# Performance work log

Hardware: AMD Instinct MI355X
Metric: run time of the kernel (lower is better)

## Reference

```python
import jax, jax.numpy as jnp
import numpy as np

K = 6            # kmer length
NF = 8192        # n_filters (> 4**K so kmer_params has shape (NF, 4, K))
M = 4 ** K       # 4096 kmers
B = 1024         # batch


def setup_inputs() -> dict:
    key = jax.random.key(0)
    k1, k2 = jax.random.split(key)
    freq = jax.random.uniform(k1, (B, M), dtype=jnp.float32)          # kmer frequencies (B, 4^k)
    kmer_params = jax.random.normal(k2, (NF, 4, K), dtype=jnp.float32)
    temperature = jnp.ones((1,), dtype=jnp.float32)
    # base-4 digits of arange(4^k), most-significant first == itertools.product order
    pos = 4 ** jnp.arange(K - 1, -1, -1)
    kmer_idcs = ((jnp.arange(M)[:, None] // pos[None, :]) % 4).astype(jnp.int32)  # (M, K)
    return {"freq": freq, "kmer_params": kmer_params,
            "temperature": temperature, "kmer_idcs": kmer_idcs}


def reference(freq, kmer_params, temperature, kmer_idcs):
    k = kmer_params.shape[-1]
    # matches[f, i] = sum_j kmer_params[f, kmer_idcs[i, j], j]
    # Advanced indexing broadcasts (M, k) indices against arange(k): result (F, M, k).
    # This replaces torch's expand-to-(F, M, 1, k) + gather + squeeze + sum(-1).
    matches = kmer_params[:, kmer_idcs, jnp.arange(k)].sum(axis=-1)   # (F, M)
    probs = jax.nn.softmax(matches / temperature, axis=1)             # softmax over kmers
    pooled = freq @ probs.T                                           # (B, F)
    profile = pooled / pooled.sum(axis=1, keepdims=True)
    return profile
```

## Files before the change

kernel.cpp:

```cpp
#include <hip/hip_runtime.h>


typedef __bf16  bf16x8 __attribute__((ext_vector_type(8)));
typedef float   f32x4  __attribute__((ext_vector_type(4)));

#define GLD16(gp, lp)                                                          \
  __builtin_amdgcn_global_load_lds(                                            \
      (const __attribute__((address_space(1))) void*)(gp),                     \
      (__attribute__((address_space(3))) void*)(lp), 16, 0, 0)

__device__ __forceinline__ short f2bf(float x) {
  unsigned u = __float_as_uint(x);
  unsigned r = (u + 0x7fffu + ((u >> 16) & 1u)) >> 16;
  return (short)r;
}

__device__ __forceinline__ float wave_max(float v) {
  #pragma unroll
  for (int off = 32; off; off >>= 1) v = fmaxf(v, __shfl_xor(v, off, 64));
  return v;
}
__device__ __forceinline__ float wave_sum(float v) {
  #pragma unroll
  for (int off = 32; off; off >>= 1) v += __shfl_xor(v, off, 64);
  return v;
}

__global__ __launch_bounds__(256) void cast_kernel(const float* __restrict__ in,
                                                   short* __restrict__ out) {
  int idx = blockIdx.x * 256 + threadIdx.x;
  float4 v = ((const float4*)in)[idx];
  short4 o;
  o.x = f2bf(v.x); o.y = f2bf(v.y); o.z = f2bf(v.z); o.w = f2bf(v.w);
  ((short4*)out)[idx] = o;
}

__global__ __launch_bounds__(256) void tables_kernel(const float* __restrict__ kp,
                                                     const float* __restrict__ temp,
                                                     float* __restrict__ E1t,
                                                     float* __restrict__ E2) {
  const int t = threadIdx.x;
  const int lane = t & 63, wave = t >> 6;
  const int f = blockIdx.x * 4 + wave;
  const float* P = kp + f * 24;
  const int d0 = (lane >> 4) & 3, d1 = (lane >> 2) & 3, d2 = lane & 3;
  const float thi = P[d0 * 6 + 0] + P[d1 * 6 + 1] + P[d2 * 6 + 2];
  const float tlo = P[d0 * 6 + 3] + P[d1 * 6 + 4] + P[d2 * 6 + 5];
  const float mxhi = wave_max(thi), mxlo = wave_max(tlo);
  const float invT = 1.0f / temp[0];
  const float e1 = __expf((thi - mxhi) * invT);
  const float e2 = __expf((tlo - mxlo) * invT);
  const float s1 = wave_sum(e1), s2 = wave_sum(e2);
  const float invZ = 1.0f / (s1 * s2);
  E1t[lane * 8192 + f] = e1 * invZ;
  E2[(size_t)f * 64 + lane] = e2;
}

__global__ __launch_bounds__(256, 2) void gemm_kernel(const short* __restrict__ A,
                                                      const float* __restrict__ E1t,
                                                      const float* __restrict__ E2,
                                                      float* __restrict__ C) {
  __shared__ short As[2][64 * 64];

  const int t = threadIdx.x;
  const int lane = t & 63, wave = t >> 6;
  const int quad = lane >> 4, l16 = lane & 15;
  const int m0 = blockIdx.y * 64;
  const int n0 = blockIdx.x * 256;
  const int wn = wave * 64;

  f32x4 acc[4][4];
  #pragma unroll
  for (int i = 0; i < 4; i++)
    #pragma unroll
    for (int j = 0; j < 4; j++) acc[i][j] = (f32x4){0.f, 0.f, 0.f, 0.f};

  int nrow[4];
  #pragma unroll
  for (int j = 0; j < 4; j++) nrow[j] = n0 + wn + j * 16 + l16;
  bf16x8 e2f[2][4];
  #pragma unroll
  for (int j = 0; j < 4; j++)
    #pragma unroll
    for (int ks = 0; ks < 2; ks++) {
      const float* p = E2 + (size_t)nrow[j] * 64 + (ks * 4 + quad) * 8;
      float4 lo = *(const float4*)p, hi = *(const float4*)(p + 4);
      bf16x8 bb;
      bb[0] = (__bf16)lo.x; bb[1] = (__bf16)lo.y;
      bb[2] = (__bf16)lo.z; bb[3] = (__bf16)lo.w;
      bb[4] = (__bf16)hi.x; bb[5] = (__bf16)hi.y;
      bb[6] = (__bf16)hi.z; bb[7] = (__bf16)hi.w;
      e2f[ks][j] = bb;
    }

  const int lane_row = lane >> 3;
  const int src_col = ((lane & 7) ^ lane_row) * 8;
  const int sw = l16 & 7;
  const int chunk = wave * 2;
  const short* Abase = A + (size_t)(m0 + lane_row) * 4096 + src_col;

  #define STG(kt, buf) do {                                                    \
    GLD16(Abase + (size_t)((chunk + 0) * 8) * 4096 + (kt) * 64,                \
          &As[buf][(chunk + 0) * 512 + lane * 8]);                             \
    GLD16(Abase + (size_t)((chunk + 1) * 8) * 4096 + (kt) * 64,                \
          &As[buf][(chunk + 1) * 512 + lane * 8]);                             \
  } while (0)

  STG(0, 0);
  float e1n[4], e1c[4];
  #pragma unroll
  for (int j = 0; j < 4; j++) e1n[j] = E1t[nrow[j]];

  const f32x4 Z4 = (f32x4){0.f, 0.f, 0.f, 0.f};

  #pragma unroll 1
  for (int kt = 0; kt < 64; ++kt) {
    const int cb = kt & 1;
    const int tn = (kt + 1 > 63) ? 63 : kt + 1;

    STG(tn, cb ^ 1);
    #pragma unroll
    for (int j = 0; j < 4; j++) e1c[j] = e1n[j];
    #pragma unroll
    for (int j = 0; j < 4; j++) e1n[j] = E1t[tn * 8192 + nrow[j]];

    asm volatile("s_waitcnt vmcnt(6)" ::: "memory");
    __builtin_amdgcn_s_barrier();

    bf16x8 a[4][2];
    #pragma unroll
    for (int i = 0; i < 4; i++)
      #pragma unroll
      for (int ks = 0; ks < 2; ks++)
        a[i][ks] = *(const bf16x8*)&As[cb][(i * 16 + l16) * 64 +
                                          (((ks * 4 + quad) ^ sw) * 8)];

    __builtin_amdgcn_s_setprio(1);
    #pragma unroll
    for (int j = 0; j < 4; j++) {
      const f32x4 s4 = (f32x4){e1c[j], e1c[j], e1c[j], e1c[j]};
      #pragma unroll
      for (int i = 0; i < 4; i++) {
        f32x4 P = __builtin_amdgcn_mfma_f32_16x16x32_bf16(a[i][0], e2f[0][j], Z4, 0, 0, 0);
        P = __builtin_amdgcn_mfma_f32_16x16x32_bf16(a[i][1], e2f[1][j], P, 0, 0, 0);
        acc[i][j] += s4 * P;
      }
    }
    __builtin_amdgcn_s_setprio(0);
    __builtin_amdgcn_s_barrier();
  }

  asm volatile("s_waitcnt vmcnt(0)" ::: "memory");

  #pragma unroll
  for (int i = 0; i < 4; i++) {
    #pragma unroll
    for (int r = 0; r < 4; r++) {
      const int brow = m0 + i * 16 + quad * 4 + r;
      float* crow = C + (size_t)brow * 8192 + n0 + wn + l16;
      #pragma unroll
      for (int j = 0; j < 4; j++) crow[j * 16] = acc[i][j][r];
    }
  }
  #undef STG
}

__global__ __launch_bounds__(256) void norm_kernel(float* __restrict__ out) {
  const int b = blockIdx.x;
  const int t = threadIdx.x;
  const int lane = t & 63, wave = t >> 6;
  __shared__ float red[4];

  float4* row = (float4*)(out + (size_t)b * 8192);
  float4 v[8];
  float s = 0.0f;
  #pragma unroll
  for (int q = 0; q < 8; q++) {
    v[q] = row[q * 256 + t];
    s += (v[q].x + v[q].y) + (v[q].z + v[q].w);
  }
  float ws = wave_sum(s);
  if (lane == 0) red[wave] = ws;
  __syncthreads();
  float tot = (red[0] + red[1]) + (red[2] + red[3]);
  float inv = 1.0f / tot;
  #pragma unroll
  for (int q = 0; q < 8; q++) {
    v[q].x *= inv; v[q].y *= inv; v[q].z *= inv; v[q].w *= inv;
    row[q * 256 + t] = v[q];
  }
}

extern "C" void kernel_launch(void* const* d_in, const int* in_sizes, int n_in,
                              void* d_out, int out_size, void* d_ws, size_t ws_size,
                              hipStream_t stream) {
  const float* freq    = (const float*)d_in[0];
  const float* kparams = (const float*)d_in[1];
  const float* temp    = (const float*)d_in[2];

  float* out = (float*)d_out;

  short* freqb = (short*)d_ws;
  float* E1t   = (float*)(freqb + (size_t)1024 * 4096);
  float* E2    = E1t + (size_t)64 * 8192;

  cast_kernel  <<<4096, 256, 0, stream>>>(freq, freqb);
  tables_kernel<<<2048, 256, 0, stream>>>(kparams, temp, E1t, E2);
  gemm_kernel  <<<dim3(32, 16), 256, 0, stream>>>(freqb, E1t, E2, out);
  norm_kernel  <<<1024, 256, 0, stream>>>(out);
}
```

Measured before the change: 159.3 us.

## Merge prep kernels and retile GEMM to register-direct loads with smaller tiles

Fuses the bf16 cast and softmax-table kernels into one launch, which removes one launch and its inter-kernel gap. The GEMM drops LDS staging and barriers. Each wave now loads its own 16-row A fragment straight from global memory into registers, with a one-step register prefetch. Tiles shrink from 64x256 to 64x64 per block, with a swizzled block index for L2 locality and launch bounds raised to 4 blocks per CU. This trades LDS reuse of A across waves for more blocks, higher occupancy and no syncs, at the cost of more redundant global loads of A and E2.

```diff
diff --git a/kernel.cpp b/kernel.cpp
--- a/kernel.cpp
+++ b/kernel.cpp
@@ -3,11 +3,6 @@
 
 typedef __bf16  bf16x8 __attribute__((ext_vector_type(8)));
 typedef float   f32x4  __attribute__((ext_vector_type(4)));
-
-#define GLD16(gp, lp)                                                          \
-  __builtin_amdgcn_global_load_lds(                                            \
-      (const __attribute__((address_space(1))) void*)(gp),                     \
-      (__attribute__((address_space(3))) void*)(lp), 16, 0, 0)
 
 __device__ __forceinline__ short f2bf(float x) {
   unsigned u = __float_as_uint(x);
@@ -26,64 +21,61 @@
   return v;
 }
 
-__global__ __launch_bounds__(256) void cast_kernel(const float* __restrict__ in,
-                                                   short* __restrict__ out) {
-  int idx = blockIdx.x * 256 + threadIdx.x;
-  float4 v = ((const float4*)in)[idx];
-  short4 o;
-  o.x = f2bf(v.x); o.y = f2bf(v.y); o.z = f2bf(v.z); o.w = f2bf(v.w);
-  ((short4*)out)[idx] = o;
+__global__ __launch_bounds__(256) void prep_kernel(const float* __restrict__ freq,
+                                                   short* __restrict__ freqb,
+                                                   const float* __restrict__ kp,
+                                                   const float* __restrict__ temp,
+                                                   float* __restrict__ E1t,
+                                                   float* __restrict__ E2) {
+  if (blockIdx.x < 4096) {
+    int idx = blockIdx.x * 256 + threadIdx.x;
+    float4 v = ((const float4*)freq)[idx];
+    short4 o;
+    o.x = f2bf(v.x); o.y = f2bf(v.y); o.z = f2bf(v.z); o.w = f2bf(v.w);
+    ((short4*)freqb)[idx] = o;
+  } else {
+    const int t = threadIdx.x;
+    const int lane = t & 63, wave = t >> 6;
+    const int f = (blockIdx.x - 4096) * 4 + wave;
+    const float* P = kp + f * 24;
+    const int d0 = (lane >> 4) & 3, d1 = (lane >> 2) & 3, d2 = lane & 3;
+    const float thi = P[d0 * 6 + 0] + P[d1 * 6 + 1] + P[d2 * 6 + 2];
+    const float tlo = P[d0 * 6 + 3] + P[d1 * 6 + 4] + P[d2 * 6 + 5];
+    const float mxhi = wave_max(thi), mxlo = wave_max(tlo);
+    const float invT = 1.0f / temp[0];
+    const float e1 = __expf((thi - mxhi) * invT);
+    const float e2 = __expf((tlo - mxlo) * invT);
+    const float s1 = wave_sum(e1), s2 = wave_sum(e2);
+    const float invZ = 1.0f / (s1 * s2);
+    E1t[lane * 8192 + f] = e1 * invZ;
+    E2[(size_t)f * 64 + lane] = e2;
+  }
 }
 
-__global__ __launch_bounds__(256) void tables_kernel(const float* __restrict__ kp,
-                                                     const float* __restrict__ temp,
-                                                     float* __restrict__ E1t,
-                                                     float* __restrict__ E2) {
-  const int t = threadIdx.x;
-  const int lane = t & 63, wave = t >> 6;
-  const int f = blockIdx.x * 4 + wave;
-  const float* P = kp + f * 24;
-  const int d0 = (lane >> 4) & 3, d1 = (lane >> 2) & 3, d2 = lane & 3;
-  const float thi = P[d0 * 6 + 0] + P[d1 * 6 + 1] + P[d2 * 6 + 2];
-  const float tlo = P[d0 * 6 + 3] + P[d1 * 6 + 4] + P[d2 * 6 + 5];
-  const float mxhi = wave_max(thi), mxlo = wave_max(tlo);
-  const float invT = 1.0f / temp[0];
-  const float e1 = __expf((thi - mxhi) * invT);
-  const float e2 = __expf((tlo - mxlo) * invT);
-  const float s1 = wave_sum(e1), s2 = wave_sum(e2);
-  const float invZ = 1.0f / (s1 * s2);
-  E1t[lane * 8192 + f] = e1 * invZ;
-  E2[(size_t)f * 64 + lane] = e2;
-}
-
-__global__ __launch_bounds__(256, 2) void gemm_kernel(const short* __restrict__ A,
+__global__ __launch_bounds__(256, 4) void gemm_kernel(const short* __restrict__ A,
                                                       const float* __restrict__ E1t,
                                                       const float* __restrict__ E2,
                                                       float* __restrict__ C) {
-  __shared__ short As[2][64 * 64];
-
   const int t = threadIdx.x;
   const int lane = t & 63, wave = t >> 6;
   const int quad = lane >> 4, l16 = lane & 15;
-  const int m0 = blockIdx.y * 64;
-  const int n0 = blockIdx.x * 256;
-  const int wn = wave * 64;
 
-  f32x4 acc[4][4];
+  const int d  = blockIdx.x;
+  const int L  = (d & 7) * 256 + (d >> 3);
+  const int m0 = (L >> 7) * 64 + wave * 16;
+  const int n0 = (L & 127) * 64;
+
+  f32x4 acc[4];
   #pragma unroll
-  for (int i = 0; i < 4; i++)
-    #pragma unroll
-    for (int j = 0; j < 4; j++) acc[i][j] = (f32x4){0.f, 0.f, 0.f, 0.f};
+  for (int j = 0; j < 4; j++) acc[j] = (f32x4){0.f, 0.f, 0.f, 0.f};
 
-  int nrow[4];
-  #pragma unroll
-  for (int j = 0; j < 4; j++) nrow[j] = n0 + wn + j * 16 + l16;
+  const int nrow0 = n0 + l16;
   bf16x8 e2f[2][4];
   #pragma unroll
   for (int j = 0; j < 4; j++)
     #pragma unroll
     for (int ks = 0; ks < 2; ks++) {
-      const float* p = E2 + (size_t)nrow[j] * 64 + (ks * 4 + quad) * 8;
+      const float* p = E2 + (size_t)(nrow0 + j * 16) * 64 + ks * 32 + quad * 8;
       float4 lo = *(const float4*)p, hi = *(const float4*)(p + 4);
       bf16x8 bb;
       bb[0] = (__bf16)lo.x; bb[1] = (__bf16)lo.y;
@@ -93,76 +85,46 @@
       e2f[ks][j] = bb;
     }
 
-  const int lane_row = lane >> 3;
-  const int src_col = ((lane & 7) ^ lane_row) * 8;
-  const int sw = l16 & 7;
-  const int chunk = wave * 2;
-  const short* Abase = A + (size_t)(m0 + lane_row) * 4096 + src_col;
+  const short* Ap = A + (size_t)(m0 + l16) * 4096 + quad * 8;
+  const float* e1p = E1t + nrow0;
 
-  #define STG(kt, buf) do {                                                    \
-    GLD16(Abase + (size_t)((chunk + 0) * 8) * 4096 + (kt) * 64,                \
-          &As[buf][(chunk + 0) * 512 + lane * 8]);                             \
-    GLD16(Abase + (size_t)((chunk + 1) * 8) * 4096 + (kt) * 64,                \
-          &As[buf][(chunk + 1) * 512 + lane * 8]);                             \
-  } while (0)
-
-  STG(0, 0);
-  float e1n[4], e1c[4];
+  bf16x8 an0 = *(const bf16x8*)(Ap);
+  bf16x8 an1 = *(const bf16x8*)(Ap + 32);
+  float e1n[4];
   #pragma unroll
-  for (int j = 0; j < 4; j++) e1n[j] = E1t[nrow[j]];
+  for (int j = 0; j < 4; j++) e1n[j] = e1p[j * 16];
 
   const f32x4 Z4 = (f32x4){0.f, 0.f, 0.f, 0.f};
 
-  #pragma unroll 1
+  #pragma unroll 4
   for (int kt = 0; kt < 64; ++kt) {
-    const int cb = kt & 1;
-    const int tn = (kt + 1 > 63) ? 63 : kt + 1;
-
-    STG(tn, cb ^ 1);
+    bf16x8 a0 = an0, a1 = an1;
+    float e1c[4];
     #pragma unroll
     for (int j = 0; j < 4; j++) e1c[j] = e1n[j];
+
+    const int tn = (kt + 1 > 63) ? 63 : kt + 1;
+    an0 = *(const bf16x8*)(Ap + tn * 64);
+    an1 = *(const bf16x8*)(Ap + tn * 64 + 32);
+    const float* ep = e1p + (size_t)tn * 8192;
     #pragma unroll
-    for (int j = 0; j < 4; j++) e1n[j] = E1t[tn * 8192 + nrow[j]];
+    for (int j = 0; j < 4; j++) e1n[j] = ep[j * 16];
 
-    asm volatile("s_waitcnt vmcnt(6)" ::: "memory");
-    __builtin_amdgcn_s_barrier();
-
-    bf16x8 a[4][2];
-    #pragma unroll
-    for (int i = 0; i < 4; i++)
-      #pragma unroll
-      for (int ks = 0; ks < 2; ks++)
-        a[i][ks] = *(const bf16x8*)&As[cb][(i * 16 + l16) * 64 +
-                                          (((ks * 4 + quad) ^ sw) * 8)];
-
-    __builtin_amdgcn_s_setprio(1);
     #pragma unroll
     for (int j = 0; j < 4; j++) {
+      f32x4 P = __builtin_amdgcn_mfma_f32_16x16x32_bf16(a0, e2f[0][j], Z4, 0, 0, 0);
+      P = __builtin_amdgcn_mfma_f32_16x16x32_bf16(a1, e2f[1][j], P, 0, 0, 0);
       const f32x4 s4 = (f32x4){e1c[j], e1c[j], e1c[j], e1c[j]};
-      #pragma unroll
-      for (int i = 0; i < 4; i++) {
-        f32x4 P = __builtin_amdgcn_mfma_f32_16x16x32_bf16(a[i][0], e2f[0][j], Z4, 0, 0, 0);
-        P = __builtin_amdgcn_mfma_f32_16x16x32_bf16(a[i][1], e2f[1][j], P, 0, 0, 0);
-        acc[i][j] += s4 * P;
-      }
+      acc[j] += s4 * P;
     }
-    __builtin_amdgcn_s_setprio(0);
-    __builtin_amdgcn_s_barrier();
   }
 
-  asm volatile("s_waitcnt vmcnt(0)" ::: "memory");
-
   #pragma unroll
-  for (int i = 0; i < 4; i++) {
+  for (int r = 0; r < 4; r++) {
+    float* crow = C + (size_t)(m0 + quad * 4 + r) * 8192 + n0 + l16;
     #pragma unroll
-    for (int r = 0; r < 4; r++) {
-      const int brow = m0 + i * 16 + quad * 4 + r;
-      float* crow = C + (size_t)brow * 8192 + n0 + wn + l16;
-      #pragma unroll
-      for (int j = 0; j < 4; j++) crow[j * 16] = acc[i][j][r];
-    }
+    for (int j = 0; j < 4; j++) crow[j * 16] = acc[j][r];
   }
-  #undef STG
 }
 
 __global__ __launch_bounds__(256) void norm_kernel(float* __restrict__ out) {
@@ -204,8 +166,7 @@
   float* E1t   = (float*)(freqb + (size_t)1024 * 4096);
   float* E2    = E1t + (size_t)64 * 8192;
 
-  cast_kernel  <<<4096, 256, 0, stream>>>(freq, freqb);
-  tables_kernel<<<2048, 256, 0, stream>>>(kparams, temp, E1t, E2);
-  gemm_kernel  <<<dim3(32, 16), 256, 0, stream>>>(freqb, E1t, E2, out);
+  prep_kernel  <<<6144, 256, 0, stream>>>(freq, freqb, kparams, temp, E1t, E2);
+  gemm_kernel  <<<2048, 256, 0, stream>>>(freqb, E1t, E2, out);
   norm_kernel  <<<1024, 256, 0, stream>>>(out);
 }
```

Result: slower. 236.5 us (+48.5%).

## Use single-wave GEMM blocks with remapped tiles and merge prep kernels

Applied to the files above, without the earlier changes.

Each GEMM workgroup becomes a single 64-thread wave computing a 64x64 output tile, so the per-iteration workgroup barriers go away. The wave now stages the whole A tile itself, and the load for the next k-step is issued after the current LDS reads. Block indices are remapped so neighbouring blocks go to different XCD groups, which is meant to improve L2 locality. The cast and table kernels are fused into one launch to save a launch. The trade-off is 2048 tiny workgroups with less shared A reuse per block, since each 64-row A tile is reused by only 64 columns instead of 256. LDS per wave also rises, which may limit occupancy.

```diff
diff --git a/kernel.cpp b/kernel.cpp
--- a/kernel.cpp
+++ b/kernel.cpp
@@ -26,48 +26,50 @@
   return v;
 }
 
-__global__ __launch_bounds__(256) void cast_kernel(const float* __restrict__ in,
-                                                   short* __restrict__ out) {
-  int idx = blockIdx.x * 256 + threadIdx.x;
-  float4 v = ((const float4*)in)[idx];
-  short4 o;
-  o.x = f2bf(v.x); o.y = f2bf(v.y); o.z = f2bf(v.z); o.w = f2bf(v.w);
-  ((short4*)out)[idx] = o;
-}
-
-__global__ __launch_bounds__(256) void tables_kernel(const float* __restrict__ kp,
-                                                     const float* __restrict__ temp,
-                                                     float* __restrict__ E1t,
-                                                     float* __restrict__ E2) {
-  const int t = threadIdx.x;
-  const int lane = t & 63, wave = t >> 6;
-  const int f = blockIdx.x * 4 + wave;
-  const float* P = kp + f * 24;
-  const int d0 = (lane >> 4) & 3, d1 = (lane >> 2) & 3, d2 = lane & 3;
-  const float thi = P[d0 * 6 + 0] + P[d1 * 6 + 1] + P[d2 * 6 + 2];
-  const float tlo = P[d0 * 6 + 3] + P[d1 * 6 + 4] + P[d2 * 6 + 5];
-  const float mxhi = wave_max(thi), mxlo = wave_max(tlo);
-  const float invT = 1.0f / temp[0];
-  const float e1 = __expf((thi - mxhi) * invT);
-  const float e2 = __expf((tlo - mxlo) * invT);
-  const float s1 = wave_sum(e1), s2 = wave_sum(e2);
-  const float invZ = 1.0f / (s1 * s2);
-  E1t[lane * 8192 + f] = e1 * invZ;
-  E2[(size_t)f * 64 + lane] = e2;
-}
-
-__global__ __launch_bounds__(256, 2) void gemm_kernel(const short* __restrict__ A,
-                                                      const float* __restrict__ E1t,
-                                                      const float* __restrict__ E2,
-                                                      float* __restrict__ C) {
+__global__ __launch_bounds__(256) void prep_kernel(const float* __restrict__ freq,
+                                                   short* __restrict__ freqb,
+                                                   const float* __restrict__ kp,
+                                                   const float* __restrict__ temp,
+                                                   float* __restrict__ E1t,
+                                                   float* __restrict__ E2) {
+  if (blockIdx.x < 4096) {
+    int idx = blockIdx.x * 256 + threadIdx.x;
+    float4 v = ((const float4*)freq)[idx];
+    short4 o;
+    o.x = f2bf(v.x); o.y = f2bf(v.y); o.z = f2bf(v.z); o.w = f2bf(v.w);
+    ((short4*)freqb)[idx] = o;
+  } else {
+    const int t = threadIdx.x;
+    const int lane = t & 63, wave = t >> 6;
+    const int f = (blockIdx.x - 4096) * 4 + wave;
+    const float* P = kp + f * 24;
+    const int d0 = (lane >> 4) & 3, d1 = (lane >> 2) & 3, d2 = lane & 3;
+    const float thi = P[d0 * 6 + 0] + P[d1 * 6 + 1] + P[d2 * 6 + 2];
+    const float tlo = P[d0 * 6 + 3] + P[d1 * 6 + 4] + P[d2 * 6 + 5];
+    const float mxhi = wave_max(thi), mxlo = wave_max(tlo);
+    const float invT = 1.0f / temp[0];
+    const float e1 = __expf((thi - mxhi) * invT);
+    const float e2 = __expf((tlo - mxlo) * invT);
+    const float s1 = wave_sum(e1), s2 = wave_sum(e2);
+    const float invZ = 1.0f / (s1 * s2);
+    E1t[lane * 8192 + f] = e1 * invZ;
+    E2[(size_t)f * 64 + lane] = e2;
+  }
+}
+
+__global__ __launch_bounds__(64, 2) void gemm_kernel(const short* __restrict__ A,
+                                                     const float* __restrict__ E1t,
+                                                     const float* __restrict__ E2,
+                                                     float* __restrict__ C) {
   __shared__ short As[2][64 * 64];
 
-  const int t = threadIdx.x;
-  const int lane = t & 63, wave = t >> 6;
+  const int lane = threadIdx.x;
   const int quad = lane >> 4, l16 = lane & 15;
-  const int m0 = blockIdx.y * 64;
-  const int n0 = blockIdx.x * 256;
-  const int wn = wave * 64;
+
+  const int d  = blockIdx.x;
+  const int L  = (d & 7) * 256 + (d >> 3);
+  const int m0 = (L >> 7) * 64;
+  const int n0 = (L & 127) * 64;
 
   f32x4 acc[4][4];
   #pragma unroll
@@ -77,7 +79,7 @@
 
   int nrow[4];
   #pragma unroll
-  for (int j = 0; j < 4; j++) nrow[j] = n0 + wn + j * 16 + l16;
+  for (int j = 0; j < 4; j++) nrow[j] = n0 + j * 16 + l16;
   bf16x8 e2f[2][4];
   #pragma unroll
   for (int j = 0; j < 4; j++)
@@ -96,14 +98,13 @@
   const int lane_row = lane >> 3;
   const int src_col = ((lane & 7) ^ lane_row) * 8;
   const int sw = l16 & 7;
-  const int chunk = wave * 2;
   const short* Abase = A + (size_t)(m0 + lane_row) * 4096 + src_col;
 
   #define STG(kt, buf) do {                                                    \
-    GLD16(Abase + (size_t)((chunk + 0) * 8) * 4096 + (kt) * 64,                \
-          &As[buf][(chunk + 0) * 512 + lane * 8]);                             \
-    GLD16(Abase + (size_t)((chunk + 1) * 8) * 4096 + (kt) * 64,                \
-          &As[buf][(chunk + 1) * 512 + lane * 8]);                             \
+    _Pragma("unroll")                                                          \
+    for (int c = 0; c < 8; c++)                                                \
+      GLD16(Abase + (size_t)(c * 8) * 4096 + (kt) * 64,                        \
+            &As[buf][c * 512 + lane * 8]);                                     \
   } while (0)
 
   STG(0, 0);
@@ -118,14 +119,8 @@
     const int cb = kt & 1;
     const int tn = (kt + 1 > 63) ? 63 : kt + 1;
 
-    STG(tn, cb ^ 1);
-    #pragma unroll
-    for (int j = 0; j < 4; j++) e1c[j] = e1n[j];
-    #pragma unroll
-    for (int j = 0; j < 4; j++) e1n[j] = E1t[tn * 8192 + nrow[j]];
-
-    asm volatile("s_waitcnt vmcnt(6)" ::: "memory");
-    __builtin_amdgcn_s_barrier();
+    asm volatile("s_waitcnt vmcnt(0)" ::: "memory");
+    __builtin_amdgcn_sched_barrier(0);
 
     bf16x8 a[4][2];
     #pragma unroll
@@ -134,6 +129,13 @@
       for (int ks = 0; ks < 2; ks++)
         a[i][ks] = *(const bf16x8*)&As[cb][(i * 16 + l16) * 64 +
                                           (((ks * 4 + quad) ^ sw) * 8)];
+
+    #pragma unroll
+    for (int j = 0; j < 4; j++) e1c[j] = e1n[j];
+
+    STG(tn, cb ^ 1);
+    #pragma unroll
+    for (int j = 0; j < 4; j++) e1n[j] = E1t[tn * 8192 + nrow[j]];
 
     __builtin_amdgcn_s_setprio(1);
     #pragma unroll
@@ -147,7 +149,6 @@
       }
     }
     __builtin_amdgcn_s_setprio(0);
-    __builtin_amdgcn_s_barrier();
   }
 
   asm volatile("s_waitcnt vmcnt(0)" ::: "memory");
@@ -157,7 +158,7 @@
     #pragma unroll
     for (int r = 0; r < 4; r++) {
       const int brow = m0 + i * 16 + quad * 4 + r;
-      float* crow = C + (size_t)brow * 8192 + n0 + wn + l16;
+      float* crow = C + (size_t)brow * 8192 + n0 + l16;
       #pragma unroll
       for (int j = 0; j < 4; j++) crow[j * 16] = acc[i][j][r];
     }
@@ -204,8 +205,7 @@
   float* E1t   = (float*)(freqb + (size_t)1024 * 4096);
   float* E2    = E1t + (size_t)64 * 8192;
 
-  cast_kernel  <<<4096, 256, 0, stream>>>(freq, freqb);
-  tables_kernel<<<2048, 256, 0, stream>>>(kparams, temp, E1t, E2);
-  gemm_kernel  <<<dim3(32, 16), 256, 0, stream>>>(freqb, E1t, E2, out);
-  norm_kernel  <<<1024, 256, 0, stream>>>(out);
-}
+  prep_kernel<<<6144, 256, 0, stream>>>(freq, freqb, kparams, temp, E1t, E2);
+  gemm_kernel<<<2048, 64, 0, stream>>>(freqb, E1t, E2, out);
+  norm_kernel<<<1024, 256, 0, stream>>>(out);
+}
```

Result: slower. 180.5 us (+13.3%).
